# Optimization experiments

Measured on AMD Instinct MI355X. Metric: run time of the kernel, lower is better.

Reference implementation:

```python
import jax, jax.numpy as jnp
import numpy as np

B, CIN, BINS, FRAMES = 8, 2, 1024, 512
NQ = 4
C = 2 * NQ          # number of quantizer channels
E = 1024            # codebook size
BETA = 0.25         # commitment cost


def conv2d(x, w, b, pad):
    y = jax.lax.conv_general_dilated(
        x, w, window_strides=(1, 1),
        padding=((pad[0], pad[0]), (pad[1], pad[1])),
        dimension_numbers=("NCHW", "OIHW", "NCHW"))
    return y + b[None, :, None, None]


def setup_inputs() -> dict:
    key = jax.random.key(0)
    ks = jax.random.split(key, 6)
    return {
        "x": jax.random.normal(ks[0], (B, CIN, BINS, FRAMES), jnp.float32),
        "conv1_w": jax.random.normal(ks[1], (C, CIN, 9, 1), jnp.float32) * 0.1,
        "conv1_b": jnp.zeros((C,), jnp.float32),
        "conv2_w": jax.random.normal(ks[2], (C, C, 9, 1), jnp.float32) * 0.05,
        "conv2_b": jnp.zeros((C,), jnp.float32),
        "skip_w": jax.random.normal(ks[3], (C, CIN, 1, 1), jnp.float32) * 0.1,
        "skip_b": jnp.zeros((C,), jnp.float32),
        "codebooks": jax.random.normal(ks[4], (C, E, BINS), jnp.float32),
    }


def reference(x, conv1_w, conv1_b, conv2_w, conv2_b, skip_w, skip_b, codebooks):
    # ResBlock projection: 2 -> 2*num_quantizers channels, (9,1) convs along bins
    h = conv2d(x, conv1_w, conv1_b, (4, 0))
    h = jax.nn.leaky_relu(h, 0.2)
    h = conv2d(h, conv2_w, conv2_b, (4, 0))
    h = h + conv2d(x, skip_w, skip_b, (0, 0))          # [B, C, BINS, F]

    # Batched VQ across all C quantizers at once.
    # Per-frame vectors: [C, N, BINS] with N = B*FRAMES
    v = jnp.transpose(h, (1, 0, 3, 2)).reshape(C, B * FRAMES, BINS)
    x2 = jnp.sum(v * v, axis=-1, keepdims=True)                     # [C,N,1]
    e2 = jnp.sum(codebooks * codebooks, axis=-1)[:, None, :]        # [C,1,E]
    d = x2 + e2 - 2.0 * jnp.einsum("cnb,ceb->cne", v, codebooks)    # [C,N,E]
    idx = jnp.argmin(d, axis=-1)                                    # [C,N]
    q = jax.vmap(lambda cb, i: cb[i])(codebooks, idx)               # [C,N,BINS]

    # VQ-VAE loss (codebook + commitment), summed over the 2Q quantizers
    sg = jax.lax.stop_gradient
    cb_loss = jnp.mean((q - sg(v)) ** 2, axis=(1, 2))
    cm_loss = jnp.mean((sg(q) - v) ** 2, axis=(1, 2))
    loss = jnp.sum(cb_loss + BETA * cm_loss)

    # straight-through estimator
    q_st = v + sg(q - v)                                            # [C,N,BINS]
    q_st = q_st.reshape(C, B, FRAMES, BINS).transpose(1, 0, 3, 2)   # [B,C,BINS,F]
    # torch loop prepends each new q: final channel order is reversed
    embedded = q_st[:, ::-1]
    return embedded, loss
```

## Files before the change

kernel.cpp:

```cpp
#include <hip/hip_runtime.h>

namespace {

constexpr int kB = 8, kCin = 2, kBins = 1024, kFrames = 512;
constexpr int kC = 8, kE = 1024, kN = kB * kFrames;

typedef _Float16 f16x8 __attribute__((ext_vector_type(8)));
typedef float f32x4 __attribute__((ext_vector_type(4)));

union HPack4 { _Float16 h[4]; uint2 u; };

__device__ inline void splitf(float v, _Float16& h, _Float16& l) {
    float a = (fabsf(v) >= 6.103515625e-05f) ? v : 0.f;
    _Float16 hh = (_Float16)a;
    h = hh;
    l = (_Float16)((v - (float)hh) * 4096.0f);
}

constexpr int BT = 32, FT = 32, XB = BT + 16, HB = BT + 8;

__global__ __launch_bounds__(256) void conv_fused_v2(
    const float* __restrict__ x,
    const float* __restrict__ w1, const float* __restrict__ b1,
    const float* __restrict__ w2, const float* __restrict__ b2,
    const float* __restrict__ wsk, const float* __restrict__ bsk,
    _Float16* __restrict__ V1, float* __restrict__ partials)
{
    __shared__ float xt[kCin][XB][33];
    __shared__ float h1t[kC][HB][33];
    __shared__ float vbuf[BT][33];
    __shared__ float w1s[kC * kCin * 9];
    __shared__ float w2s[kC * kC][12];
    __shared__ float wsks[kC * kCin];
    __shared__ float b1s[kC], b2s[kC], bsks[kC];
    __shared__ float reds[256];

    const int t = threadIdx.x;
    const int bt = blockIdx.x, ft = blockIdx.y, bb = blockIdx.z;
    const int bs = bt * BT, f0 = ft * FT;
    _Float16* V2 = V1 + (size_t)33554432;

    for (int i = t; i < kC * kCin * 9; i += 256) w1s[i] = w1[i];
    for (int i = t; i < 768; i += 256) {
        int cc = i / 12, k = i % 12;
        w2s[cc][k] = (k < 9) ? w2[cc * 9 + k] : 0.f;
    }
    if (t < kC * kCin) wsks[t] = wsk[t];
    if (t < kC) { b1s[t] = b1[t]; b2s[t] = b2[t]; bsks[t] = bsk[t]; }

    for (int i = t; i < kCin * XB * FT; i += 256) {
        int fi = i % FT, xb = (i / FT) % XB, ci = i / (FT * XB);
        int gb = bs - 8 + xb;
        float v = 0.f;
        if (gb >= 0 && gb < kBins)
            v = x[((bb * kCin + ci) * kBins + gb) * kFrames + f0 + fi];
        xt[ci][xb][fi] = v;
    }
    __syncthreads();

    const int fi = t & 31;
    const int r = t >> 5;

    for (int q = 0; q < 5; q++) {
        float a8[8];
        #pragma unroll
        for (int jj = 0; jj < 8; jj++) a8[jj] = b1s[r];
        #pragma unroll
        for (int ci = 0; ci < kCin; ci++) {
            float w[16];
            #pragma unroll
            for (int k = 0; k < 16; k++) w[k] = xt[ci][q * 8 + k][fi];
            const float* wp = &w1s[(r * kCin + ci) * 9];
            #pragma unroll
            for (int jj = 0; jj < 8; jj++)
                #pragma unroll
                for (int k = 0; k < 9; k++)
                    a8[jj] += w[jj + k] * wp[k];
        }
        #pragma unroll
        for (int jj = 0; jj < 8; jj++) {
            int hb = q * 8 + jj;
            int gb = bs - 4 + hb;
            float v = (gb >= 0 && gb < kBins) ? (a8[jj] > 0.f ? a8[jj] : 0.2f * a8[jj]) : 0.f;
            h1t[r][hb][fi] = v;
        }
    }
    __syncthreads();

    float acc[8][4];
    #pragma unroll
    for (int c = 0; c < 8; c++)
        #pragma unroll
        for (int j = 0; j < 4; j++) acc[c][j] = b2s[c] + bsks[c];

    for (int ci = 0; ci < 8; ci++) {
        float w[12];
        #pragma unroll
        for (int k = 0; k < 12; k++) w[k] = h1t[ci][r * 4 + k][fi];
        #pragma unroll
        for (int c = 0; c < 8; c++) {
            const float4* wp4 = (const float4*)&w2s[c * 8 + ci][0];
            float4 wA = wp4[0], wB = wp4[1], wC = wp4[2];
            float wk[9] = {wA.x, wA.y, wA.z, wA.w, wB.x, wB.y, wB.z, wB.w, wC.x};
            #pragma unroll
            for (int j = 0; j < 4; j++) {
                float s = 0.f;
                #pragma unroll
                for (int k = 0; k < 9; k++) s += w[j + k] * wk[k];
                acc[c][j] += s;
            }
        }
    }
    #pragma unroll
    for (int j = 0; j < 4; j++) {
        float x0 = xt[0][r * 4 + j + 8][fi];
        float x1 = xt[1][r * 4 + j + 8][fi];
        #pragma unroll
        for (int c = 0; c < 8; c++)
            acc[c][j] += x0 * wsks[c * 2] + x1 * wsks[c * 2 + 1];
    }

    float sq = 0.f;
    #pragma unroll
    for (int c = 0; c < 8; c++)
        #pragma unroll
        for (int j = 0; j < 4; j++) sq += acc[c][j] * acc[c][j];

    const int rr = t >> 3, q = t & 7;
    for (int c = 0; c < 8; c++) {
        __syncthreads();
        #pragma unroll
        for (int j = 0; j < 4; j++) vbuf[r * 4 + j][fi] = acc[c][j];
        __syncthreads();
        HPack4 ph, pl;
        #pragma unroll
        for (int j = 0; j < 4; j++) {
            float v = vbuf[q * 4 + j][rr];
            splitf(v, ph.h[j], pl.h[j]);
        }
        const int n = bb * kFrames + f0 + rr;
        const size_t off = ((size_t)(c * kN + n)) * kBins + bs + q * 4;
        *(uint2*)&V1[off] = ph.u;
        *(uint2*)&V2[off] = pl.u;
    }

    reds[t] = sq;
    __syncthreads();
    for (int off = 128; off > 0; off >>= 1) {
        if (t < off) reds[t] += reds[t + off];
        __syncthreads();
    }
    if (t == 0) {
        int blin = (bb * gridDim.y + blockIdx.y) * gridDim.x + blockIdx.x;
        partials[blin] = reds[0];
    }
}

__global__ __launch_bounds__(256) void cbsplit_e2(
    const float* __restrict__ cb, _Float16* __restrict__ B1,
    float* __restrict__ e2, unsigned long long* __restrict__ pk)
{
    const int gid = blockIdx.x * 256 + threadIdx.x;
    if (gid < kC * kN) pk[gid] = ~0ull;

    const int gw = gid >> 6;
    const int lane = threadIdx.x & 63;
    _Float16* B2 = B1 + (size_t)8388608;
    const float* row = cb + (size_t)gw * kBins;
    float s = 0.f;
    #pragma unroll
    for (int j = 0; j < 4; j++) {
        float4 v = *(const float4*)&row[lane * 4 + j * 256];
        s += v.x * v.x + v.y * v.y + v.z * v.z + v.w * v.w;
        HPack4 ph, pl;
        splitf(v.x, ph.h[0], pl.h[0]);
        splitf(v.y, ph.h[1], pl.h[1]);
        splitf(v.z, ph.h[2], pl.h[2]);
        splitf(v.w, ph.h[3], pl.h[3]);
        size_t off = (size_t)gw * kBins + lane * 4 + j * 256;
        *(uint2*)&B1[off] = ph.u;
        *(uint2*)&B2[off] = pl.u;
    }
    #pragma unroll
    for (int off = 32; off > 0; off >>= 1) s += __shfl_down(s, off);
    if (lane == 0) e2[gw] = s;
}

__global__ __launch_bounds__(256, 2) void dist_mfma(
    const _Float16* __restrict__ V1, const _Float16* __restrict__ B1p,
    const float* __restrict__ e2, unsigned long long* __restrict__ pk)
{
    __shared__ char smem[2 * 32768 + 2048];

    const int t = threadIdx.x;
    const int bidx = blockIdx.x;
    const int ch = bidx & 7;
    const int eh = (bidx >> 3) & 1;
    const int n0 = (bidx >> 4) * 128;
    const int w = t >> 6, lane = t & 63;
    const int l15 = lane & 15, kc4 = lane >> 4;
    const int wm = w >> 1, we = w & 1;

    float* lds_e2 = (float*)(smem + 65536);
    {
        const float* e2c = e2 + ch * kE + eh * 512;
        float a = e2c[t], b = e2c[t + 256];
        lds_e2[t] = a;
        lds_e2[t + 256] = b;
    }

    const _Float16* srcA[4];
    const _Float16* srcB[4];
    int dstoff[4];
    #pragma unroll
    for (int i = 0; i < 4; i++) {
        int ci = w * 256 + i * 64 + lane;
        int row = ci >> 3, slot = ci & 7;
        int g = slot ^ (row & 7);
        int p = g >> 2, kc = g & 3;
        srcA[i] = V1 + (size_t)p * 33554432 + ((size_t)(ch * kN + n0 + row)) * kBins + kc * 8;
        srcB[i] = B1p + (size_t)p * 8388608 + ((size_t)(ch * kE + row)) * kBins + kc * 8;
        dstoff[i] = (w * 256 + i * 64) * 16;
    }

    const int rowA = wm * 64 + l15;
    const int rowB = we * 64 + l15;
    const int baseA1 = rowA * 128 + ((kc4) ^ (rowA & 7)) * 16;
    const int baseA2 = rowA * 128 + ((4 + kc4) ^ (rowA & 7)) * 16;
    const int baseB1 = 16384 + rowB * 128 + ((kc4) ^ (rowB & 7)) * 16;
    const int baseB2 = 16384 + rowB * 128 + ((4 + kc4) ^ (rowB & 7)) * 16;

    float rm[16];
    int ri[16];
    #pragma unroll
    for (int s = 0; s < 16; s++) { rm[s] = 3.4e38f; ri[s] = 0; }

    typedef const __attribute__((address_space(1))) void gsrc_t;
    typedef __attribute__((address_space(3))) void gdst_t;

    auto issue = [&](int jj) {
        const int k0 = (jj & 31) * 32;
        const size_t etoff = (size_t)(eh * 4 + (jj >> 5)) * 128 * kBins + k0;
        char* nb = smem + (jj & 1) * 32768;
        #pragma unroll
        for (int i = 0; i < 4; i++)
            __builtin_amdgcn_global_load_lds((gsrc_t*)(srcA[i] + k0), (gdst_t*)(nb + dstoff[i]), 16, 0, 0);
        #pragma unroll
        for (int i = 0; i < 4; i++)
            __builtin_amdgcn_global_load_lds((gsrc_t*)(srcB[i] + etoff), (gdst_t*)(nb + 16384 + dstoff[i]), 16, 0, 0);
    };

    f32x4 hi[4][4], lo[4][4];
    #pragma unroll
    for (int mi = 0; mi < 4; mi++)
        #pragma unroll
        for (int ei = 0; ei < 4; ei++) {
            hi[mi][ei] = (f32x4){0.f, 0.f, 0.f, 0.f};
            lo[mi][ei] = (f32x4){0.f, 0.f, 0.f, 0.f};
        }

    __syncthreads();

    issue(0);

    #pragma unroll 1
    for (int et = 0; et < 4; et++) {
        #pragma unroll 1
        for (int ks = 0; ks < 32; ks++) {
            const int j = et * 32 + ks;
            asm volatile("s_waitcnt vmcnt(0)\n\ts_barrier" ::: "memory");
            if (j < 127) issue(j + 1);

            const char* buf = smem + (j & 1) * 32768;
            f16x8 a1[4], a2[4], b1f[4], b2f[4];
            #pragma unroll
            for (int mi = 0; mi < 4; mi++) {
                a1[mi] = *(const f16x8*)(buf + baseA1 + mi * 2048);
                a2[mi] = *(const f16x8*)(buf + baseA2 + mi * 2048);
            }
            #pragma unroll
            for (int ei = 0; ei < 4; ei++) {
                b1f[ei] = *(const f16x8*)(buf + baseB1 + ei * 2048);
                b2f[ei] = *(const f16x8*)(buf + baseB2 + ei * 2048);
            }
            __builtin_amdgcn_s_setprio(1);
            #pragma unroll
            for (int mi = 0; mi < 4; mi++)
                #pragma unroll
                for (int ei = 0; ei < 4; ei++) {
                    hi[mi][ei] = __builtin_amdgcn_mfma_f32_16x16x32_f16(a1[mi], b1f[ei], hi[mi][ei], 0, 0, 0);
                    lo[mi][ei] = __builtin_amdgcn_mfma_f32_16x16x32_f16(a1[mi], b2f[ei], lo[mi][ei], 0, 0, 0);
                    lo[mi][ei] = __builtin_amdgcn_mfma_f32_16x16x32_f16(a2[mi], b1f[ei], lo[mi][ei], 0, 0, 0);
                }
            __builtin_amdgcn_s_setprio(0);
        }

        #pragma unroll
        for (int ei = 0; ei < 4; ei++) {
            const int eloc = et * 128 + we * 64 + ei * 16 + l15;
            const float ev = lds_e2[eloc];
            const int eix = eh * 512 + eloc;
            #pragma unroll
            for (int mi = 0; mi < 4; mi++) {
                f32x4 dot4 = hi[mi][ei] + lo[mi][ei] * (1.0f / 4096.0f);
                #pragma unroll
                for (int rr = 0; rr < 4; rr++) {
                    float d = ev - 2.0f * dot4[rr];
                    int s = mi * 4 + rr;
                    if (d < rm[s]) { rm[s] = d; ri[s] = eix; }
                }
                hi[mi][ei] = (f32x4){0.f, 0.f, 0.f, 0.f};
                lo[mi][ei] = (f32x4){0.f, 0.f, 0.f, 0.f};
            }
        }
    }

    #pragma unroll
    for (int m = 1; m < 16; m <<= 1) {
        #pragma unroll
        for (int s = 0; s < 16; s++) {
            float ov = __shfl_xor(rm[s], m);
            int oi = __shfl_xor(ri[s], m);
            if (ov < rm[s] || (ov == rm[s] && oi < ri[s])) { rm[s] = ov; ri[s] = oi; }
        }
    }

    float* mv = (float*)smem;
    int* miv = (int*)(smem + 1024);
    __syncthreads();
    if (l15 == 0) {
        #pragma unroll
        for (int s = 0; s < 16; s++) {
            int mi = s >> 2, rr = s & 3;
            int rloc = wm * 64 + mi * 16 + (lane >> 4) * 4 + rr;
            mv[rloc * 2 + we] = rm[s];
            miv[rloc * 2 + we] = ri[s];
        }
    }
    __syncthreads();
    if (t < 128) {
        float v0 = mv[t * 2], v1 = mv[t * 2 + 1];
        int i0 = miv[t * 2], i1 = miv[t * 2 + 1];
        bool take1 = (v1 < v0) || (v1 == v0 && i1 < i0);
        float bv = take1 ? v1 : v0;
        int bi = take1 ? i1 : i0;
        unsigned int u = __float_as_uint(bv);
        unsigned int su = (u & 0x80000000u) ? ~u : (u ^ 0x80000000u);
        unsigned long long packed = ((unsigned long long)su << 32) | (unsigned int)bi;
        atomicMin(&pk[ch * kN + n0 + t], packed);
    }
}

__global__ __launch_bounds__(256) void gather_pk(
    const float* __restrict__ cb, const unsigned long long* __restrict__ pk,
    const float* __restrict__ partials, float* __restrict__ out,
    float* __restrict__ loss)
{
    const int t = threadIdx.x;
    const int lane = t & 63, q = t >> 6;
    const int b = blockIdx.x;
    const int cp = b & 7;
    const int bt = (b >> 3) & 63;
    const int ftile = (b >> 9) & 7;
    const int bb = b >> 12;
    const int co = (kC - 1) - cp;
    const int f = ftile * 64 + lane;
    const int n = bb * kFrames + f;
    const int e = (int)(unsigned int)(pk[cp * kN + n] & 0xFFFFFFFFull);
    const int bin0 = bt * 16 + q * 4;
    const float4 v4 = *(const float4*)&cb[((size_t)cp * kE + e) * kBins + bin0];
    const size_t base = ((size_t)(bb * kC + co) * kBins + bin0) * kFrames + f;
    out[base] = v4.x;
    out[base + kFrames] = v4.y;
    out[base + 2 * (size_t)kFrames] = v4.z;
    out[base + 3 * (size_t)kFrames] = v4.w;

    if (b == 32767) {
        __shared__ float reds[256];
        float s = 0.f;
        for (int i = t; i < kC * kN; i += 256) {
            unsigned int su = (unsigned int)(pk[i] >> 32);
            unsigned int u = (su & 0x80000000u) ? (su ^ 0x80000000u) : ~su;
            s += __uint_as_float(u);
        }
        for (int i = t; i < 4096; i += 256) s += partials[i];
        reds[t] = s;
        __syncthreads();
        for (int off = 128; off > 0; off >>= 1) {
            if (t < off) reds[t] += reds[t + off];
            __syncthreads();
        }
        if (t == 0) loss[0] = 1.25f * reds[0] / (float)(kN * kBins);
    }
}

}

extern "C" void kernel_launch(void* const* d_in, const int* in_sizes, int n_in,
                              void* d_out, int out_size, void* d_ws, size_t ws_size,
                              hipStream_t stream)
{
    const float* x   = (const float*)d_in[0];
    const float* w1  = (const float*)d_in[1];
    const float* b1  = (const float*)d_in[2];
    const float* w2  = (const float*)d_in[3];
    const float* b2  = (const float*)d_in[4];
    const float* wsk = (const float*)d_in[5];
    const float* bsk = (const float*)d_in[6];
    const float* cb  = (const float*)d_in[7];
    float* out = (float*)d_out;
    char* ws = (char*)d_ws;

    _Float16* B1 = (_Float16*)ws;
    float* e2                  = (float*)(ws + 33554432);
    unsigned long long* pk     = (unsigned long long*)(ws + 33554432 + 32768);
    float* partials            = (float*)(ws + 33554432 + 32768 + 262144);
    _Float16* V1 = (_Float16*)d_out;

    conv_fused_v2<<<dim3(kBins / BT, kFrames / FT, kB), 256, 0, stream>>>(
        x, w1, b1, w2, b2, wsk, bsk, V1, partials);
    cbsplit_e2<<<(kC * kE) / 4, 256, 0, stream>>>(cb, B1, e2, pk);
    dist_mfma<<<dim3(512), 256, 0, stream>>>(V1, B1, e2, pk);
    gather_pk<<<dim3(32768), 256, 0, stream>>>(cb, pk, partials, out,
                                               out + (size_t)kC * kBins * kN);
}
```

Measured before the change: 418.3 us.

## Restructure conv kernel into register-resident per-thread bin strips with packed stores

Rewrites the fused conv kernel so each thread holds a 24-bin input window and all 8 first-layer channels in registers, computing 8 output bins per channel without shared-memory staging of x or h1. Outputs are split into fp16 hi/lo pairs, packed into a shared tile, and written as 16-byte vector stores along bins, with one barrier instead of a barrier pair per channel. The tile grows to 64 frames, so the grid and the partial-sum count halve. The cost is much higher register pressure (h1[8][16] plus windows), which could lower occupancy or cause spills.

New measurement: 592.1 us. 41.6% more time.

```diff
diff --git a/kernel.cpp b/kernel.cpp
--- a/kernel.cpp
+++ b/kernel.cpp
@@ -4,11 +4,13 @@
 
 constexpr int kB = 8, kCin = 2, kBins = 1024, kFrames = 512;
 constexpr int kC = 8, kE = 1024, kN = kB * kFrames;
+constexpr int kNPart = 2048;
 
 typedef _Float16 f16x8 __attribute__((ext_vector_type(8)));
 typedef float f32x4 __attribute__((ext_vector_type(4)));
 
 union HPack4 { _Float16 h[4]; uint2 u; };
+union HPack2 { _Float16 h[2]; unsigned int u; };
 
 __device__ inline void splitf(float v, _Float16& h, _Float16& l) {
     float a = (fabsf(v) >= 6.103515625e-05f) ? v : 0.f;
@@ -17,131 +19,127 @@
     l = (_Float16)((v - (float)hh) * 4096.0f);
 }
 
-constexpr int BT = 32, FT = 32, XB = BT + 16, HB = BT + 8;
-
-__global__ __launch_bounds__(256) void conv_fused_v2(
+__global__ __launch_bounds__(256) void conv_fused_v3(
     const float* __restrict__ x,
     const float* __restrict__ w1, const float* __restrict__ b1,
     const float* __restrict__ w2, const float* __restrict__ b2,
     const float* __restrict__ wsk, const float* __restrict__ bsk,
     _Float16* __restrict__ V1, float* __restrict__ partials)
 {
-    __shared__ float xt[kCin][XB][33];
-    __shared__ float h1t[kC][HB][33];
-    __shared__ float vbuf[BT][33];
-    __shared__ float w1s[kC * kCin * 9];
-    __shared__ float w2s[kC * kC][12];
-    __shared__ float wsks[kC * kCin];
-    __shared__ float b1s[kC], b2s[kC], bsks[kC];
+    __shared__ unsigned int vtile[8][64][36];
+    __shared__ float w1s[144];
+    __shared__ float w2s[64 * 12];
+    __shared__ float wsks[16];
+    __shared__ float b1s[8], b2s[8], bsks[8];
     __shared__ float reds[256];
 
     const int t = threadIdx.x;
-    const int bt = blockIdx.x, ft = blockIdx.y, bb = blockIdx.z;
-    const int bs = bt * BT, f0 = ft * FT;
-    _Float16* V2 = V1 + (size_t)33554432;
-
-    for (int i = t; i < kC * kCin * 9; i += 256) w1s[i] = w1[i];
+    const int w = t >> 6, l = t & 63;
+    const int C32 = blockIdx.x * 32;
+    const int s = C32 + w * 8;
+    const int f0 = blockIdx.y * 64;
+    const int bb = blockIdx.z;
+
+    if (t < 144) w1s[t] = w1[t];
     for (int i = t; i < 768; i += 256) {
         int cc = i / 12, k = i % 12;
-        w2s[cc][k] = (k < 9) ? w2[cc * 9 + k] : 0.f;
-    }
-    if (t < kC * kCin) wsks[t] = wsk[t];
-    if (t < kC) { b1s[t] = b1[t]; b2s[t] = b2[t]; bsks[t] = bsk[t]; }
-
-    for (int i = t; i < kCin * XB * FT; i += 256) {
-        int fi = i % FT, xb = (i / FT) % XB, ci = i / (FT * XB);
-        int gb = bs - 8 + xb;
-        float v = 0.f;
-        if (gb >= 0 && gb < kBins)
-            v = x[((bb * kCin + ci) * kBins + gb) * kFrames + f0 + fi];
-        xt[ci][xb][fi] = v;
-    }
-    __syncthreads();
-
-    const int fi = t & 31;
-    const int r = t >> 5;
-
-    for (int q = 0; q < 5; q++) {
-        float a8[8];
-        #pragma unroll
-        for (int jj = 0; jj < 8; jj++) a8[jj] = b1s[r];
-        #pragma unroll
-        for (int ci = 0; ci < kCin; ci++) {
-            float w[16];
-            #pragma unroll
-            for (int k = 0; k < 16; k++) w[k] = xt[ci][q * 8 + k][fi];
-            const float* wp = &w1s[(r * kCin + ci) * 9];
-            #pragma unroll
-            for (int jj = 0; jj < 8; jj++)
+        w2s[cc * 12 + k] = (k < 9) ? w2[cc * 9 + k] : 0.f;
+    }
+    if (t < 16) wsks[t] = wsk[t];
+    if (t < 8) { b1s[t] = b1[t]; b2s[t] = b2[t]; bsks[t] = bsk[t]; }
+    __syncthreads();
+
+    float xw[2][24];
+    #pragma unroll
+    for (int ci = 0; ci < 2; ci++)
+        #pragma unroll
+        for (int jx = 0; jx < 24; jx++) {
+            int gb = s - 8 + jx;
+            xw[ci][jx] = (gb >= 0 && gb < kBins)
+                ? x[((size_t)(bb * kCin + ci) * kBins + gb) * kFrames + f0 + l]
+                : 0.f;
+        }
+
+    float h1[8][16];
+    #pragma unroll
+    for (int cm = 0; cm < 8; cm++) {
+        float wp[18];
+        #pragma unroll
+        for (int i = 0; i < 18; i++) wp[i] = w1s[cm * 18 + i];
+        #pragma unroll
+        for (int j = 0; j < 16; j++) {
+            int gbh = s - 4 + j;
+            float a = b1s[cm];
+            #pragma unroll
+            for (int ci = 0; ci < 2; ci++)
                 #pragma unroll
                 for (int k = 0; k < 9; k++)
-                    a8[jj] += w[jj + k] * wp[k];
-        }
-        #pragma unroll
-        for (int jj = 0; jj < 8; jj++) {
-            int hb = q * 8 + jj;
-            int gb = bs - 4 + hb;
-            float v = (gb >= 0 && gb < kBins) ? (a8[jj] > 0.f ? a8[jj] : 0.2f * a8[jj]) : 0.f;
-            h1t[r][hb][fi] = v;
-        }
-    }
-    __syncthreads();
-
-    float acc[8][4];
-    #pragma unroll
-    for (int c = 0; c < 8; c++)
-        #pragma unroll
-        for (int j = 0; j < 4; j++) acc[c][j] = b2s[c] + bsks[c];
-
-    for (int ci = 0; ci < 8; ci++) {
-        float w[12];
-        #pragma unroll
-        for (int k = 0; k < 12; k++) w[k] = h1t[ci][r * 4 + k][fi];
-        #pragma unroll
-        for (int c = 0; c < 8; c++) {
-            const float4* wp4 = (const float4*)&w2s[c * 8 + ci][0];
+                    a += xw[ci][j + k] * wp[ci * 9 + k];
+            h1[cm][j] = (gbh >= 0 && gbh < kBins) ? (a > 0.f ? a : 0.2f * a) : 0.f;
+        }
+    }
+
+    float xs0[8], xs1[8];
+    #pragma unroll
+    for (int jj = 0; jj < 8; jj++) { xs0[jj] = xw[0][jj + 8]; xs1[jj] = xw[1][jj + 8]; }
+
+    float sq = 0.f;
+    #pragma unroll
+    for (int c = 0; c < 8; c++) {
+        float acc[8];
+        #pragma unroll
+        for (int jj = 0; jj < 8; jj++) acc[jj] = b2s[c] + bsks[c];
+        #pragma unroll
+        for (int ci = 0; ci < 8; ci++) {
+            const float4* wp4 = (const float4*)&w2s[(c * 8 + ci) * 12];
             float4 wA = wp4[0], wB = wp4[1], wC = wp4[2];
             float wk[9] = {wA.x, wA.y, wA.z, wA.w, wB.x, wB.y, wB.z, wB.w, wC.x};
             #pragma unroll
-            for (int j = 0; j < 4; j++) {
-                float s = 0.f;
+            for (int jj = 0; jj < 8; jj++) {
+                float sci = 0.f;
                 #pragma unroll
-                for (int k = 0; k < 9; k++) s += w[j + k] * wk[k];
-                acc[c][j] += s;
+                for (int k = 0; k < 9; k++) sci += h1[ci][jj + k] * wk[k];
+                acc[jj] += sci;
             }
         }
-    }
-    #pragma unroll
-    for (int j = 0; j < 4; j++) {
-        float x0 = xt[0][r * 4 + j + 8][fi];
-        float x1 = xt[1][r * 4 + j + 8][fi];
-        #pragma unroll
-        for (int c = 0; c < 8; c++)
-            acc[c][j] += x0 * wsks[c * 2] + x1 * wsks[c * 2 + 1];
-    }
-
-    float sq = 0.f;
-    #pragma unroll
-    for (int c = 0; c < 8; c++)
-        #pragma unroll
-        for (int j = 0; j < 4; j++) sq += acc[c][j] * acc[c][j];
-
-    const int rr = t >> 3, q = t & 7;
-    for (int c = 0; c < 8; c++) {
-        __syncthreads();
-        #pragma unroll
-        for (int j = 0; j < 4; j++) vbuf[r * 4 + j][fi] = acc[c][j];
-        __syncthreads();
-        HPack4 ph, pl;
-        #pragma unroll
-        for (int j = 0; j < 4; j++) {
-            float v = vbuf[q * 4 + j][rr];
-            splitf(v, ph.h[j], pl.h[j]);
-        }
-        const int n = bb * kFrames + f0 + rr;
-        const size_t off = ((size_t)(c * kN + n)) * kBins + bs + q * 4;
-        *(uint2*)&V1[off] = ph.u;
-        *(uint2*)&V2[off] = pl.u;
+        unsigned int vals[8];
+        #pragma unroll
+        for (int jj = 0; jj < 8; jj++) {
+            acc[jj] += xs0[jj] * wsks[c * 2] + xs1[jj] * wsks[c * 2 + 1];
+            sq += acc[jj] * acc[jj];
+            HPack2 p;
+            splitf(acc[jj], p.h[0], p.h[1]);
+            vals[jj] = p.u;
+        }
+        *(uint4*)&vtile[c][l][w * 8] =
+            make_uint4(vals[0], vals[1], vals[2], vals[3]);
+        *(uint4*)&vtile[c][l][w * 8 + 4] =
+            make_uint4(vals[4], vals[5], vals[6], vals[7]);
+    }
+    __syncthreads();
+
+    _Float16* V2 = V1 + (size_t)33554432;
+    #pragma unroll
+    for (int it = 0; it < 2; it++) {
+        const int p = it * 256 + t;
+        const int c = p >> 6, f = p & 63;
+        const size_t vbase = ((size_t)(c * kN + bb * kFrames + f0 + f)) * kBins + C32;
+        #pragma unroll
+        for (int g = 0; g < 4; g++) {
+            uint4 a = *(const uint4*)&vtile[c][f][g * 8];
+            uint4 b = *(const uint4*)&vtile[c][f][g * 8 + 4];
+            uint4 h4, l4;
+            h4.x = (a.x & 0xffffu) | (a.y << 16);
+            h4.y = (a.z & 0xffffu) | (a.w << 16);
+            h4.z = (b.x & 0xffffu) | (b.y << 16);
+            h4.w = (b.z & 0xffffu) | (b.w << 16);
+            l4.x = (a.x >> 16) | (a.y & 0xffff0000u);
+            l4.y = (a.z >> 16) | (a.w & 0xffff0000u);
+            l4.z = (b.x >> 16) | (b.y & 0xffff0000u);
+            l4.w = (b.z >> 16) | (b.w & 0xffff0000u);
+            *(uint4*)&V1[vbase + g * 8] = h4;
+            *(uint4*)&V2[vbase + g * 8] = l4;
+        }
     }
 
     reds[t] = sq;
@@ -151,7 +149,7 @@
         __syncthreads();
     }
     if (t == 0) {
-        int blin = (bb * gridDim.y + blockIdx.y) * gridDim.x + blockIdx.x;
+        int blin = (blockIdx.z * gridDim.y + blockIdx.y) * gridDim.x + blockIdx.x;
         partials[blin] = reds[0];
     }
 }
@@ -383,7 +381,7 @@
             unsigned int u = (su & 0x80000000u) ? (su ^ 0x80000000u) : ~su;
             s += __uint_as_float(u);
         }
-        for (int i = t; i < 4096; i += 256) s += partials[i];
+        for (int i = t; i < kNPart; i += 256) s += partials[i];
         reds[t] = s;
         __syncthreads();
         for (int off = 128; off > 0; off >>= 1) {
@@ -417,7 +415,7 @@
     float* partials            = (float*)(ws + 33554432 + 32768 + 262144);
     _Float16* V1 = (_Float16*)d_out;
 
-    conv_fused_v2<<<dim3(kBins / BT, kFrames / FT, kB), 256, 0, stream>>>(
+    conv_fused_v3<<<dim3(32, 8, 8), 256, 0, stream>>>(
         x, w1, b1, w2, b2, wsk, bsk, V1, partials);
     cbsplit_e2<<<(kC * kE) / 4, 256, 0, stream>>>(cb, B1, e2, pk);
     dist_mfma<<<dim3(512), 256, 0, stream>>>(V1, B1, e2, pk);
```

## Enlarge dist_mfma block to 256 rows and triple-buffer LDS loads

Applied to the files above, without the earlier changes.

Doubles the row tile per block (512 threads, 256 query rows), so each codebook tile loaded into LDS is reused by twice as many rows, and halves the grid. Replaces double buffering with a three-stage ring and prefetch distance two, waiting with a partial vmcnt so loads overlap MFMA work. LDS use rises to about 146KB per block, limiting residency to one block per CU, and the final reduction is resized accordingly.

Result: faster. 409.8 us (-2.0%).

```diff
diff --git a/kernel.cpp b/kernel.cpp
--- a/kernel.cpp
+++ b/kernel.cpp
@@ -186,49 +186,53 @@
     if (lane == 0) e2[gw] = s;
 }
 
-__global__ __launch_bounds__(256, 2) void dist_mfma(
+__global__ __launch_bounds__(512, 2) void dist_mfma(
     const _Float16* __restrict__ V1, const _Float16* __restrict__ B1p,
     const float* __restrict__ e2, unsigned long long* __restrict__ pk)
 {
-    __shared__ char smem[2 * 32768 + 2048];
+    __shared__ char smem[3 * 49152 + 2048];
 
     const int t = threadIdx.x;
     const int bidx = blockIdx.x;
     const int ch = bidx & 7;
     const int eh = (bidx >> 3) & 1;
-    const int n0 = (bidx >> 4) * 128;
+    const int n0 = (bidx >> 4) * 256;
     const int w = t >> 6, lane = t & 63;
     const int l15 = lane & 15, kc4 = lane >> 4;
     const int wm = w >> 1, we = w & 1;
 
-    float* lds_e2 = (float*)(smem + 65536);
-    {
-        const float* e2c = e2 + ch * kE + eh * 512;
-        float a = e2c[t], b = e2c[t + 256];
-        lds_e2[t] = a;
-        lds_e2[t + 256] = b;
-    }
+    float* lds_e2 = (float*)(smem + 147456);
+    lds_e2[t] = e2[ch * kE + eh * 512 + t];
 
     const _Float16* srcA[4];
-    const _Float16* srcB[4];
-    int dstoff[4];
+    int dstA[4];
     #pragma unroll
     for (int i = 0; i < 4; i++) {
-        int ci = w * 256 + i * 64 + lane;
+        int ci = i * 512 + t;
         int row = ci >> 3, slot = ci & 7;
         int g = slot ^ (row & 7);
         int p = g >> 2, kc = g & 3;
         srcA[i] = V1 + (size_t)p * 33554432 + ((size_t)(ch * kN + n0 + row)) * kBins + kc * 8;
+        dstA[i] = ci * 16;
+    }
+    const _Float16* srcB[2];
+    int dstB[2];
+    #pragma unroll
+    for (int i = 0; i < 2; i++) {
+        int bi = i * 512 + t;
+        int row = bi >> 3, slot = bi & 7;
+        int g = slot ^ (row & 7);
+        int p = g >> 2, kc = g & 3;
         srcB[i] = B1p + (size_t)p * 8388608 + ((size_t)(ch * kE + row)) * kBins + kc * 8;
-        dstoff[i] = (w * 256 + i * 64) * 16;
+        dstB[i] = 32768 + bi * 16;
     }
 
     const int rowA = wm * 64 + l15;
     const int rowB = we * 64 + l15;
     const int baseA1 = rowA * 128 + ((kc4) ^ (rowA & 7)) * 16;
     const int baseA2 = rowA * 128 + ((4 + kc4) ^ (rowA & 7)) * 16;
-    const int baseB1 = 16384 + rowB * 128 + ((kc4) ^ (rowB & 7)) * 16;
-    const int baseB2 = 16384 + rowB * 128 + ((4 + kc4) ^ (rowB & 7)) * 16;
+    const int baseB1 = 32768 + rowB * 128 + ((kc4) ^ (rowB & 7)) * 16;
+    const int baseB2 = 32768 + rowB * 128 + ((4 + kc4) ^ (rowB & 7)) * 16;
 
     float rm[16];
     int ri[16];
@@ -238,40 +242,50 @@
     typedef const __attribute__((address_space(1))) void gsrc_t;
     typedef __attribute__((address_space(3))) void gdst_t;
 
-    auto issue = [&](int jj) {
+    auto issue = [&](int jj, int bw) {
         const int k0 = (jj & 31) * 32;
         const size_t etoff = (size_t)(eh * 4 + (jj >> 5)) * 128 * kBins + k0;
-        char* nb = smem + (jj & 1) * 32768;
+        char* nb = smem + bw * 49152;
         #pragma unroll
         for (int i = 0; i < 4; i++)
-            __builtin_amdgcn_global_load_lds((gsrc_t*)(srcA[i] + k0), (gdst_t*)(nb + dstoff[i]), 16, 0, 0);
-        #pragma unroll
-        for (int i = 0; i < 4; i++)
-            __builtin_amdgcn_global_load_lds((gsrc_t*)(srcB[i] + etoff), (gdst_t*)(nb + 16384 + dstoff[i]), 16, 0, 0);
+            __builtin_amdgcn_global_load_lds((gsrc_t*)(srcA[i] + k0), (gdst_t*)(nb + dstA[i]), 16, 0, 0);
+        #pragma unroll
+        for (int i = 0; i < 2; i++)
+            __builtin_amdgcn_global_load_lds((gsrc_t*)(srcB[i] + etoff), (gdst_t*)(nb + dstB[i]), 16, 0, 0);
     };
 
-    f32x4 hi[4][4], lo[4][4];
-    #pragma unroll
-    for (int mi = 0; mi < 4; mi++)
-        #pragma unroll
-        for (int ei = 0; ei < 4; ei++) {
-            hi[mi][ei] = (f32x4){0.f, 0.f, 0.f, 0.f};
-            lo[mi][ei] = (f32x4){0.f, 0.f, 0.f, 0.f};
-        }
-
-    __syncthreads();
-
-    issue(0);
+    __syncthreads();
+
+    issue(0, 0);
+    issue(1, 1);
+    int bread = 0, bwrite = 2;
 
     #pragma unroll 1
     for (int et = 0; et < 4; et++) {
+        f32x4 hi[4][4], lo[4][4];
+        #pragma unroll
+        for (int mi = 0; mi < 4; mi++)
+            #pragma unroll
+            for (int ei = 0; ei < 4; ei++) {
+                hi[mi][ei] = (f32x4){0.f, 0.f, 0.f, 0.f};
+                lo[mi][ei] = (f32x4){0.f, 0.f, 0.f, 0.f};
+            }
+
         #pragma unroll 1
         for (int ks = 0; ks < 32; ks++) {
             const int j = et * 32 + ks;
-            asm volatile("s_waitcnt vmcnt(0)\n\ts_barrier" ::: "memory");
-            if (j < 127) issue(j + 1);
-
-            const char* buf = smem + (j & 1) * 32768;
+            if (j < 127)
+                asm volatile("s_waitcnt vmcnt(6)\n\ts_barrier" ::: "memory");
+            else
+                asm volatile("s_waitcnt vmcnt(0)\n\ts_barrier" ::: "memory");
+            if (j < 126) {
+                issue(j + 2, bwrite);
+                bwrite = (bwrite == 2) ? 0 : bwrite + 1;
+            }
+
+            const char* buf = smem + bread * 49152;
+            bread = (bread == 2) ? 0 : bread + 1;
+
             f16x8 a1[4], a2[4], b1f[4], b2f[4];
             #pragma unroll
             for (int mi = 0; mi < 4; mi++) {
@@ -309,8 +323,6 @@
                     int s = mi * 4 + rr;
                     if (d < rm[s]) { rm[s] = d; ri[s] = eix; }
                 }
-                hi[mi][ei] = (f32x4){0.f, 0.f, 0.f, 0.f};
-                lo[mi][ei] = (f32x4){0.f, 0.f, 0.f, 0.f};
             }
         }
     }
@@ -326,7 +338,7 @@
     }
 
     float* mv = (float*)smem;
-    int* miv = (int*)(smem + 1024);
+    int* miv = (int*)(smem + 2048);
     __syncthreads();
     if (l15 == 0) {
         #pragma unroll
@@ -338,7 +350,7 @@
         }
     }
     __syncthreads();
-    if (t < 128) {
+    if (t < 256) {
         float v0 = mv[t * 2], v1 = mv[t * 2 + 1];
         int i0 = miv[t * 2], i1 = miv[t * 2 + 1];
         bool take1 = (v1 < v0) || (v1 == v0 && i1 < i0);
@@ -420,7 +432,7 @@
     conv_fused_v2<<<dim3(kBins / BT, kFrames / FT, kB), 256, 0, stream>>>(
         x, w1, b1, w2, b2, wsk, bsk, V1, partials);
     cbsplit_e2<<<(kC * kE) / 4, 256, 0, stream>>>(cb, B1, e2, pk);
-    dist_mfma<<<dim3(512), 256, 0, stream>>>(V1, B1, e2, pk);
+    dist_mfma<<<dim3(256), 512, 0, stream>>>(V1, B1, e2, pk);
     gather_pk<<<dim3(32768), 256, 0, stream>>>(cb, pk, partials, out,
                                                out + (size_t)kC * kBins * kN);
 }
```
